# Performance work log

Measured on AMD Instinct MI355X. Metric: run time of the kernel, lower is better.

## Reference

```python
import jax, jax.numpy as jnp
import numpy as np


def _binop(ei, ej):
    # diagonal linear recurrence combine: (a_i, b_i) * (a_j, b_j) -> (a_j*a_i, a_j*b_i + b_j)
    ai, bi = ei
    aj, bj = ej
    return aj * ai, aj * bi + bj


def setup_inputs() -> dict:
    key = jax.random.key(0)
    ks = jax.random.split(key, 9)
    B_, T, D_in, D_out, N = 16, 2048, 512, 512, 512
    inp = {
        "input": jax.random.normal(ks[0], (B_, T, D_in), dtype=jnp.float32),
        "D": jax.random.normal(ks[1], (D_out, D_in), dtype=jnp.float32) / np.sqrt(D_in),
        "nu_log": jax.random.normal(ks[2], (N,), dtype=jnp.float32),
        "theta_log": jax.random.normal(ks[3], (N,), dtype=jnp.float32),
        "gamma_log": jax.random.normal(ks[4], (N,), dtype=jnp.float32),
        "B_re": jax.random.normal(ks[5], (N, D_in), dtype=jnp.float32) / np.sqrt(2 * D_in),
        "B_im": jax.random.normal(ks[6], (N, D_in), dtype=jnp.float32) / np.sqrt(2 * D_in),
        "C_re": jax.random.normal(ks[7], (D_out, N), dtype=jnp.float32) / np.sqrt(N),
        "C_im": jax.random.normal(ks[8], (D_out, N), dtype=jnp.float32) / np.sqrt(N),
    }
    return inp


def reference(input, D, nu_log, theta_log, gamma_log, B_re, B_im, C_re, C_im):
    # ss_params
    lam_abs = jnp.exp(-jnp.exp(nu_log))                      # [N]
    lam_phase = jnp.exp(theta_log)                           # [N]
    lam = lam_abs * (jnp.cos(lam_phase) + 1j * jnp.sin(lam_phase))  # complex [N]
    gamma = jnp.exp(gamma_log)                               # [N]
    Bc = (B_re + 1j * B_im) * gamma[:, None]                 # [N, D_in]
    Cc = C_re + 1j * C_im                                    # [D_out, N]

    # input projection: Bu_elements [batch, T, N] (complex)
    Bu = input.astype(Bc.dtype) @ Bc.T
    lam_el = jnp.broadcast_to(lam, Bu.shape)

    # parallel associative scan over time axis (initial state is zero)
    _, states = jax.lax.associative_scan(_binop, (lam_el, Bu), axis=1)

    # readout
    y = jnp.real(states @ Cc.T) + input @ D.T                # [batch, T, D_out]
    return y
```

## Files before the change

kernel.cpp:

```cpp
#include <hip/hip_runtime.h>
#include <hip/hip_fp16.h>

typedef _Float16 f16;
typedef __attribute__((ext_vector_type(8))) _Float16 f16x8;
typedef __attribute__((ext_vector_type(2))) _Float16 f16x2;
typedef __attribute__((ext_vector_type(16))) float f32x16;

#define B_SZ 16
#define T_SZ 2048
#define DIN 512
#define DOUT 512
#define N_SZ 512
#define M_SZ (B_SZ * T_SZ)
#define NCHUNK 16
#define LCHUNK 128

__device__ __forceinline__ void gload_lds16(const void* g, void* l) {
  __builtin_amdgcn_global_load_lds(
      (const __attribute__((address_space(1))) void*)g,
      (__attribute__((address_space(3))) void*)l, 16, 0, 0);
}


__global__ void prep_all(const float* __restrict__ nu_log,
                         const float* __restrict__ theta_log,
                         const float* __restrict__ gamma_log,
                         const float* __restrict__ B_re, const float* __restrict__ B_im,
                         const float* __restrict__ C_re, const float* __restrict__ C_im,
                         const float* __restrict__ Dm, const float* __restrict__ input,
                         float2* __restrict__ lam2, float2* __restrict__ lamL2,
                         f16* __restrict__ W1, f16* __restrict__ W2,
                         f16* __restrict__ A2) {
  int b = blockIdx.x;
  if (b < 2) {
    int n = b * 256 + threadIdx.x;
    float nu = expf(nu_log[n]);
    float ph = expf(theta_log[n]);
    float la = expf(-nu);
    lam2[n] = make_float2(la * cosf(ph), la * sinf(ph));
    float laL = expf(-nu * (float)LCHUNK);
    float phL = ph * (float)LCHUNK;
    lamL2[n] = make_float2(laL * cosf(phL), laL * sinf(phL));
  } else if (b < 2 + 2048) {
    int tid = (b - 2) * 256 + threadIdx.x;
    int np = tid >> 9;
    int d = tid & 511;
    int n = np >> 1;
    float g = expf(gamma_log[n]);
    const float* src = (np & 1) ? B_im : B_re;
    W1[(size_t)np * 512 + d] = (f16)(src[(size_t)n * 512 + d] * g);
  } else if (b < 2 + 2048 + 3072) {
    int tid = (b - 2050) * 256 + threadIdx.x;
    int j = tid / 1536;
    int k = tid - j * 1536;
    float v;
    if (k < 512)       v =  C_re[(size_t)j * 512 + k];
    else if (k < 1024) v = -C_im[(size_t)j * 512 + (k - 512)];
    else               v =  Dm[(size_t)j * 512 + (k - 1024)];
    W2[(size_t)j * 1536 + k] = (f16)v;
  } else {
    int tid = (b - 5122) * 256 + threadIdx.x;
    int m = tid >> 6;
    int d0 = (tid & 63) << 3;
    const float4* p = (const float4*)(input + (size_t)m * DIN + d0);
    float4 a = p[0], c = p[1];
    f16x8 h;
    h[0] = (f16)a.x; h[1] = (f16)a.y; h[2] = (f16)a.z; h[3] = (f16)a.w;
    h[4] = (f16)c.x; h[5] = (f16)c.y; h[6] = (f16)c.z; h[7] = (f16)c.w;
    *(f16x8*)(A2 + (size_t)m * 1536 + 1024 + d0) = h;
  }
}


__global__ void scan_a(const f16* __restrict__ Bu, const float2* __restrict__ lam2,
                       float2* __restrict__ S) {
  int tid = blockIdx.x * 256 + threadIdx.x;
  int n = tid & 511;
  int c = (tid >> 9) & (NCHUNK - 1);
  int b = tid >> 13;
  float2 l = lam2[n];
  const unsigned* bu = (const unsigned*)Bu + (size_t)(b * T_SZ + c * LCHUNK) * 512 + n;
  float sre = 0.f, sim = 0.f;
#pragma unroll 8
  for (int t = 0; t < LCHUNK; ++t) {
    unsigned u = bu[(size_t)t * 512];
    f16x2 h = __builtin_bit_cast(f16x2, u);
    float nre = l.x * sre - l.y * sim + (float)h.x;
    sim = l.x * sim + l.y * sre + (float)h.y;
    sre = nre;
  }
  S[(size_t)(b * NCHUNK + c) * 512 + n] = make_float2(sre, sim);
}

__global__ void scan_b(const float2* __restrict__ S, const float2* __restrict__ lamL2,
                       float2* __restrict__ Carry) {
  int tid = blockIdx.x * 256 + threadIdx.x;
  int n = tid & 511;
  int b = tid >> 9;
  float2 lL = lamL2[n];
  float cre = 0.f, cim = 0.f;
  for (int c = 0; c < NCHUNK; ++c) {
    size_t idx = (size_t)(b * NCHUNK + c) * 512 + n;
    Carry[idx] = make_float2(cre, cim);
    float2 s = S[idx];
    float nre = lL.x * cre - lL.y * cim + s.x;
    cim = lL.x * cim + lL.y * cre + s.y;
    cre = nre;
  }
}

__global__ void scan_c(const f16* __restrict__ Bu, const float2* __restrict__ lam2,
                       const float2* __restrict__ Carry, f16* __restrict__ A2) {
  int tid = blockIdx.x * 256 + threadIdx.x;
  int n = tid & 511;
  int c = (tid >> 9) & (NCHUNK - 1);
  int b = tid >> 13;
  float2 l = lam2[n];
  float2 car = Carry[(size_t)(b * NCHUNK + c) * 512 + n];
  float sre = car.x, sim = car.y;
  int m0 = b * T_SZ + c * LCHUNK;
  const unsigned* bu = (const unsigned*)Bu + (size_t)m0 * 512 + n;
  f16* outre = A2 + (size_t)m0 * 1536 + n;
#pragma unroll 4
  for (int t = 0; t < LCHUNK; ++t) {
    unsigned u = bu[(size_t)t * 512];
    f16x2 h = __builtin_bit_cast(f16x2, u);
    float nre = l.x * sre - l.y * sim + (float)h.x;
    sim = l.x * sim + l.y * sre + (float)h.y;
    sre = nre;
    outre[(size_t)t * 1536] = (f16)sre;
    outre[(size_t)t * 1536 + 512] = (f16)sim;
  }
}


template <typename CT>
__global__ __launch_bounds__(512, 2) void gemm_ring(
    const f16* __restrict__ A, int lda,
    const f16* __restrict__ Bm, int ldb,
    CT* __restrict__ C, int ldc, int K, int nxt) {
  extern __shared__ f16 smem[];
  const int tid = threadIdx.x;
  const int lane = tid & 63;
  const int wid = tid >> 6;
  const int wr = wid >> 2;
  const int wc = wid & 3;
  const int r32 = lane & 31;
  const int khalf = lane >> 5;
  const int key = (r32 & 3) ^ ((r32 >> 2) & 3);

  const int nwg = gridDim.x;
  const int id = blockIdx.x;
  const int swz = (id & 7) * (nwg >> 3) + (id >> 3);
  const int m0 = (swz / nxt) * 256;
  const int n0 = (swz % nxt) * 256;

  const int srow = tid >> 2;
  const int scol = ((tid & 3) ^ (srow & 3) ^ ((srow >> 2) & 3)) * 8;
  const int NG = K >> 5;

  f32x16 acc[4][2];
#pragma unroll
  for (int i = 0; i < 4; ++i)
#pragma unroll
    for (int j = 0; j < 2; ++j)
#pragma unroll
      for (int r = 0; r < 16; ++r) acc[i][j][r] = 0.f;

  auto stage = [&](int g) {
    f16* dst = smem + (g & 3) * 16384 + tid * 8;
    const f16* gA = A + (size_t)(m0 + srow) * lda + g * 32 + scol;
    const f16* gB = Bm + (size_t)(n0 + srow) * ldb + g * 32 + scol;
    gload_lds16(gA, dst);
    gload_lds16(gA + (size_t)128 * lda, dst + 4096);
    gload_lds16(gB, dst + 8192);
    gload_lds16(gB + (size_t)128 * ldb, dst + 12288);
  };

  f16x8 af[4][2], bf[2][2];
  auto ldfrags = [&](int g) {
    const f16* sa = smem + (g & 3) * 16384 + (wr * 128) * 32;
    const f16* sb = smem + (g & 3) * 16384 + 8192 + (wc * 64) * 32;
#pragma unroll
    for (int mi = 0; mi < 4; ++mi)
#pragma unroll
      for (int k = 0; k < 2; ++k)
        af[mi][k] = *(const f16x8*)(sa + (mi * 32 + r32) * 32 +
                                    (((k * 2 + khalf) ^ key) * 8));
#pragma unroll
    for (int ni = 0; ni < 2; ++ni)
#pragma unroll
      for (int k = 0; k < 2; ++k)
        bf[ni][k] = *(const f16x8*)(sb + (ni * 32 + r32) * 32 +
                                    (((k * 2 + khalf) ^ key) * 8));
  };

  stage(0);
  stage(1);
  stage(2);
  asm volatile("s_waitcnt vmcnt(4)" ::: "memory");
  __builtin_amdgcn_sched_barrier(0);
  __builtin_amdgcn_s_barrier();
  __builtin_amdgcn_sched_barrier(0);
  ldfrags(0);

  for (int g = 0; g < NG; ++g) {
    asm volatile("s_waitcnt lgkmcnt(0)" ::: "memory");
    __builtin_amdgcn_sched_barrier(0);
    if (g + 3 < NG) stage(g + 3);
    __builtin_amdgcn_s_setprio(1);
#pragma unroll
    for (int k = 0; k < 2; ++k)
#pragma unroll
      for (int mi = 0; mi < 4; ++mi)
#pragma unroll
        for (int ni = 0; ni < 2; ++ni)
          acc[mi][ni] = __builtin_amdgcn_mfma_f32_32x32x16_f16(
              af[mi][k], bf[ni][k], acc[mi][ni], 0, 0, 0);
    __builtin_amdgcn_s_setprio(0);
    __builtin_amdgcn_sched_barrier(0);
    if (g + 1 < NG) {
      if (g + 3 < NG)
        asm volatile("s_waitcnt vmcnt(4)" ::: "memory");
      else if (g + 2 < NG)
        asm volatile("s_waitcnt vmcnt(0)" ::: "memory");
      ldfrags(g + 1);
    }
    __builtin_amdgcn_sched_barrier(0);
    __builtin_amdgcn_s_barrier();
    __builtin_amdgcn_sched_barrier(0);
  }

#pragma unroll
  for (int mi = 0; mi < 4; ++mi)
#pragma unroll
    for (int ni = 0; ni < 2; ++ni)
#pragma unroll
      for (int r = 0; r < 16; ++r) {
        int row = m0 + wr * 128 + mi * 32 + (r & 3) + ((r >> 2) * 8) + khalf * 4;
        int col = n0 + wc * 64 + ni * 32 + r32;
        C[(size_t)row * ldc + col] = (CT)acc[mi][ni][r];
      }
}


extern "C" void kernel_launch(void* const* d_in, const int* in_sizes, int n_in,
                              void* d_out, int out_size, void* d_ws, size_t ws_size,
                              hipStream_t stream) {
  const float* input = (const float*)d_in[0];
  const float* Dmat = (const float*)d_in[1];
  const float* nu_log = (const float*)d_in[2];
  const float* theta_log = (const float*)d_in[3];
  const float* gamma_log = (const float*)d_in[4];
  const float* B_re = (const float*)d_in[5];
  const float* B_im = (const float*)d_in[6];
  const float* C_re = (const float*)d_in[7];
  const float* C_im = (const float*)d_in[8];
  float* y = (float*)d_out;

  char* ws = (char*)d_ws;
  size_t off = 0;
  auto alloc = [&](size_t bytes) {
    void* p = ws + off;
    off = (off + bytes + 255) & ~(size_t)255;
    return p;
  };
  float2* lam2 = (float2*)alloc(N_SZ * sizeof(float2));
  float2* lamL2 = (float2*)alloc(N_SZ * sizeof(float2));
  f16* W1 = (f16*)alloc((size_t)2 * N_SZ * DIN * 2);
  f16* W2 = (f16*)alloc((size_t)DOUT * 1536 * 2);
  f16* A2 = (f16*)alloc((size_t)M_SZ * 1536 * 2);
  f16* Bu = (f16*)alloc((size_t)M_SZ * 2 * N_SZ * 2);
  float2* S = (float2*)alloc((size_t)B_SZ * NCHUNK * N_SZ * sizeof(float2));
  float2* Carry = (float2*)alloc((size_t)B_SZ * NCHUNK * N_SZ * sizeof(float2));

  const int shmem = 131072;
  {
    auto* g16 = gemm_ring<f16>;
    auto* g32 = gemm_ring<float>;
    hipFuncSetAttribute((const void*)g16,
                        hipFuncAttributeMaxDynamicSharedMemorySize, shmem);
    hipFuncSetAttribute((const void*)g32,
                        hipFuncAttributeMaxDynamicSharedMemorySize, shmem);
  }

  prep_all<<<13314, 256, 0, stream>>>(nu_log, theta_log, gamma_log, B_re, B_im,
                                      C_re, C_im, Dmat, input, lam2, lamL2, W1, W2, A2);

  gemm_ring<f16><<<512, 512, shmem, stream>>>(A2 + 1024, 1536, W1, 512, Bu, 1024, 512, 4);

  scan_a<<<(B_SZ * NCHUNK * N_SZ) / 256, 256, 0, stream>>>(Bu, lam2, S);
  scan_b<<<(B_SZ * N_SZ) / 256, 256, 0, stream>>>(S, lamL2, Carry);
  scan_c<<<(B_SZ * NCHUNK * N_SZ) / 256, 256, 0, stream>>>(Bu, lam2, Carry, A2);

  gemm_ring<float><<<256, 512, shmem, stream>>>(A2, 1536, W2, 1536, y, 512, 1536, 2);
}
```

Before: 171.9 us.

## Shrink GEMM tile to 256x128 and double-buffer fragment registers

Shrinks the GEMM block tile from 256x256 to 256x128, with each of the eight waves now owning a 64x64 sub-tile. This doubles the grid size and cuts the shared-memory ring to 96KB. The main loop is unrolled by two with ping-pong register fragments, so LDS loads for the next k-step are issued before the current MFMAs and partially awaited with lgkmcnt. The aim is to hide LDS latency and improve occupancy and wave balance, at the cost of lower arithmetic intensity per tile and more global B traffic.

```diff
diff --git a/kernel.cpp b/kernel.cpp
--- a/kernel.cpp
+++ b/kernel.cpp
@@ -135,7 +135,7 @@
 
 
 template <typename CT>
-__global__ __launch_bounds__(512, 2) void gemm_ring(
+__global__ __launch_bounds__(512, 2) void gemm_pipe(
     const f16* __restrict__ A, int lda,
     const f16* __restrict__ Bm, int ldb,
     CT* __restrict__ C, int ldc, int K, int nxt) {
@@ -143,8 +143,8 @@
   const int tid = threadIdx.x;
   const int lane = tid & 63;
   const int wid = tid >> 6;
-  const int wr = wid >> 2;
-  const int wc = wid & 3;
+  const int wr = wid >> 1;
+  const int wc = wid & 1;
   const int r32 = lane & 31;
   const int khalf = lane >> 5;
   const int key = (r32 & 3) ^ ((r32 >> 2) & 3);
@@ -153,36 +153,34 @@
   const int id = blockIdx.x;
   const int swz = (id & 7) * (nwg >> 3) + (id >> 3);
   const int m0 = (swz / nxt) * 256;
-  const int n0 = (swz % nxt) * 256;
+  const int n0 = (swz % nxt) * 128;
 
   const int srow = tid >> 2;
   const int scol = ((tid & 3) ^ (srow & 3) ^ ((srow >> 2) & 3)) * 8;
   const int NG = K >> 5;
 
-  f32x16 acc[4][2];
-#pragma unroll
-  for (int i = 0; i < 4; ++i)
+  f32x16 acc[2][2];
+#pragma unroll
+  for (int i = 0; i < 2; ++i)
 #pragma unroll
     for (int j = 0; j < 2; ++j)
 #pragma unroll
       for (int r = 0; r < 16; ++r) acc[i][j][r] = 0.f;
 
   auto stage = [&](int g) {
-    f16* dst = smem + (g & 3) * 16384 + tid * 8;
+    f16* dst = smem + (g & 3) * 12288 + tid * 8;
     const f16* gA = A + (size_t)(m0 + srow) * lda + g * 32 + scol;
     const f16* gB = Bm + (size_t)(n0 + srow) * ldb + g * 32 + scol;
     gload_lds16(gA, dst);
     gload_lds16(gA + (size_t)128 * lda, dst + 4096);
     gload_lds16(gB, dst + 8192);
-    gload_lds16(gB + (size_t)128 * ldb, dst + 12288);
   };
 
-  f16x8 af[4][2], bf[2][2];
-  auto ldfrags = [&](int g) {
-    const f16* sa = smem + (g & 3) * 16384 + (wr * 128) * 32;
-    const f16* sb = smem + (g & 3) * 16384 + 8192 + (wc * 64) * 32;
-#pragma unroll
-    for (int mi = 0; mi < 4; ++mi)
+  auto ldfrags = [&](int g, f16x8 (&af)[2][2], f16x8 (&bf)[2][2]) {
+    const f16* sa = smem + (g & 3) * 12288 + (wr * 64) * 32;
+    const f16* sb = smem + (g & 3) * 12288 + 8192 + (wc * 64) * 32;
+#pragma unroll
+    for (int mi = 0; mi < 2; ++mi)
 #pragma unroll
       for (int k = 0; k < 2; ++k)
         af[mi][k] = *(const f16x8*)(sa + (mi * 32 + r32) * 32 +
@@ -195,49 +193,58 @@
                                     (((k * 2 + khalf) ^ key) * 8));
   };
 
+  f16x8 afA[2][2], bfA[2][2], afB[2][2], bfB[2][2];
+
+  auto body = [&](int g, f16x8 (&uaf)[2][2], f16x8 (&ubf)[2][2],
+                  f16x8 (&naf)[2][2], f16x8 (&nbf)[2][2]) {
+    if (g + 1 < NG) ldfrags(g + 1, naf, nbf);
+    if (g + 3 < NG) stage(g + 3);
+    __builtin_amdgcn_sched_barrier(0);
+    if (g + 1 < NG)
+      asm volatile("s_waitcnt lgkmcnt(8)" ::: "memory");
+    else
+      asm volatile("s_waitcnt lgkmcnt(0)" ::: "memory");
+    __builtin_amdgcn_sched_barrier(0);
+    __builtin_amdgcn_s_setprio(1);
+#pragma unroll
+    for (int k = 0; k < 2; ++k)
+#pragma unroll
+      for (int mi = 0; mi < 2; ++mi)
+#pragma unroll
+        for (int ni = 0; ni < 2; ++ni)
+          acc[mi][ni] = __builtin_amdgcn_mfma_f32_32x32x16_f16(
+              uaf[mi][k], ubf[ni][k], acc[mi][ni], 0, 0, 0);
+    __builtin_amdgcn_s_setprio(0);
+    __builtin_amdgcn_sched_barrier(0);
+    if (g + 3 < NG)
+      asm volatile("s_waitcnt vmcnt(3)" ::: "memory");
+    else if (g + 2 < NG)
+      asm volatile("s_waitcnt vmcnt(0)" ::: "memory");
+    __builtin_amdgcn_s_barrier();
+    __builtin_amdgcn_sched_barrier(0);
+  };
+
   stage(0);
   stage(1);
   stage(2);
-  asm volatile("s_waitcnt vmcnt(4)" ::: "memory");
+  asm volatile("s_waitcnt vmcnt(3)" ::: "memory");
   __builtin_amdgcn_sched_barrier(0);
   __builtin_amdgcn_s_barrier();
   __builtin_amdgcn_sched_barrier(0);
-  ldfrags(0);
-
-  for (int g = 0; g < NG; ++g) {
-    asm volatile("s_waitcnt lgkmcnt(0)" ::: "memory");
-    __builtin_amdgcn_sched_barrier(0);
-    if (g + 3 < NG) stage(g + 3);
-    __builtin_amdgcn_s_setprio(1);
-#pragma unroll
-    for (int k = 0; k < 2; ++k)
-#pragma unroll
-      for (int mi = 0; mi < 4; ++mi)
-#pragma unroll
-        for (int ni = 0; ni < 2; ++ni)
-          acc[mi][ni] = __builtin_amdgcn_mfma_f32_32x32x16_f16(
-              af[mi][k], bf[ni][k], acc[mi][ni], 0, 0, 0);
-    __builtin_amdgcn_s_setprio(0);
-    __builtin_amdgcn_sched_barrier(0);
-    if (g + 1 < NG) {
-      if (g + 3 < NG)
-        asm volatile("s_waitcnt vmcnt(4)" ::: "memory");
-      else if (g + 2 < NG)
-        asm volatile("s_waitcnt vmcnt(0)" ::: "memory");
-      ldfrags(g + 1);
-    }
-    __builtin_amdgcn_sched_barrier(0);
-    __builtin_amdgcn_s_barrier();
-    __builtin_amdgcn_sched_barrier(0);
-  }
-
-#pragma unroll
-  for (int mi = 0; mi < 4; ++mi)
+  ldfrags(0, afA, bfA);
+
+  for (int g = 0; g < NG; g += 2) {
+    body(g, afA, bfA, afB, bfB);
+    body(g + 1, afB, bfB, afA, bfA);
+  }
+
+#pragma unroll
+  for (int mi = 0; mi < 2; ++mi)
 #pragma unroll
     for (int ni = 0; ni < 2; ++ni)
 #pragma unroll
       for (int r = 0; r < 16; ++r) {
-        int row = m0 + wr * 128 + mi * 32 + (r & 3) + ((r >> 2) * 8) + khalf * 4;
+        int row = m0 + wr * 64 + mi * 32 + (r & 3) + ((r >> 2) * 8) + khalf * 4;
         int col = n0 + wc * 64 + ni * 32 + r32;
         C[(size_t)row * ldc + col] = (CT)acc[mi][ni][r];
       }
@@ -274,10 +281,10 @@
   float2* S = (float2*)alloc((size_t)B_SZ * NCHUNK * N_SZ * sizeof(float2));
   float2* Carry = (float2*)alloc((size_t)B_SZ * NCHUNK * N_SZ * sizeof(float2));
 
-  const int shmem = 131072;
+  const int shmem = 98304;
   {
-    auto* g16 = gemm_ring<f16>;
-    auto* g32 = gemm_ring<float>;
+    auto* g16 = gemm_pipe<f16>;
+    auto* g32 = gemm_pipe<float>;
     hipFuncSetAttribute((const void*)g16,
                         hipFuncAttributeMaxDynamicSharedMemorySize, shmem);
     hipFuncSetAttribute((const void*)g32,
@@ -287,11 +294,11 @@
   prep_all<<<13314, 256, 0, stream>>>(nu_log, theta_log, gamma_log, B_re, B_im,
                                       C_re, C_im, Dmat, input, lam2, lamL2, W1, W2, A2);
 
-  gemm_ring<f16><<<512, 512, shmem, stream>>>(A2 + 1024, 1536, W1, 512, Bu, 1024, 512, 4);
+  gemm_pipe<f16><<<1024, 512, shmem, stream>>>(A2 + 1024, 1536, W1, 512, Bu, 1024, 512, 8);
 
   scan_a<<<(B_SZ * NCHUNK * N_SZ) / 256, 256, 0, stream>>>(Bu, lam2, S);
   scan_b<<<(B_SZ * N_SZ) / 256, 256, 0, stream>>>(S, lamL2, Carry);
   scan_c<<<(B_SZ * NCHUNK * N_SZ) / 256, 256, 0, stream>>>(Bu, lam2, Carry, A2);
 
-  gemm_ring<float><<<256, 512, shmem, stream>>>(A2, 1536, W2, 1536, y, 512, 1536, 2);
-}
+  gemm_pipe<float><<<512, 512, shmem, stream>>>(A2, 1536, W2, 1536, y, 512, 1536, 4);
+}
```

After: 188.8 us. 9.8% more time.
